# Kernel optimization log

Measured on AMD Instinct MI355X. Metric: run time of the kernel, lower is better.

The kernel has to match this reference:

```python
import jax, jax.numpy as jnp
import numpy as np
from functools import partial

NF, CD, NB = 64, 32, 3  # num_feat, chan_dyn, num_block


def _conv(x, w, b, stride, pad):
    out = jax.lax.conv_general_dilated(x, w, (stride, stride), ((pad, pad), (pad, pad)),
                                       dimension_numbers=('NCHW', 'OIHW', 'NCHW'))
    return out + b[None, :, None, None]


def _condition_tp(x, w1, b1, w2, b2, w3, b3):
    # ZeroPad2d(1) + conv(stride=2, pad=0) == conv with pad=1, stride=2
    h = jax.nn.relu(_conv(x, w1, b1, 2, 1))   # 7x7
    h = jax.nn.relu(_conv(h, w2, b2, 2, 1))   # 3x3
    h = jax.nn.relu(_conv(h, w3, b3, 2, 1))   # 3x3
    return h.mean(axis=(2, 3))                # [N, 32]


def _lstm_step(x, h, c, w):
    # ConvLSTMCell with 1x1 kernel on 1x1 spatial maps -> plain matmul
    gates = jnp.concatenate([x, h], axis=1) @ w.T        # [N, 4*NF]
    i, f, o, g = jnp.split(gates, 4, axis=1)
    c = jax.nn.sigmoid(f) * c + jax.nn.sigmoid(i) * jnp.tanh(g)
    h = jax.nn.sigmoid(o) * jnp.tanh(c)
    return h, c


def _forward(x, cond, rep_w1, rep_w2, lstm_fw_w, lstm_bw_w, lstm_conv_w, lstm_conv_b,
             conv_first_w, conv_first_b, bc1_w, bc1_b, bc2_w, bc2_b, bc3_w, bc3_b,
             bscale_w, bscale_b, bshift_w, bshift_b, bshare1_w, bshare1_b, bdyn1_w,
             bshare2_w, bshare2_b, bdyn2_w, fc1_w, fc1_b, fc2_w, fc2_b, fc3_w, fc3_b,
             fconv_w, fconv_b, fscale_w, fscale_b, fshift_w, fshift_b):
    lrelu = partial(jax.nn.leaky_relu, negative_slope=0.1)
    b = x.shape[0]
    # conv_represent -> [B, CD*NF] -> pseudo-batch [CD*B, NF] (spatial is 1x1)
    rep = (lrelu(cond @ rep_w1.T) @ rep_w2.T).reshape(b * CD, NF)
    # bidirectional ConvLSTM over 2*NB steps of the same input
    hf = cf = hb = cb = jnp.zeros_like(rep)
    ws_for, ws_back = [], []
    for _ in range(NB * 2):
        hf, cf = _lstm_step(rep, hf, cf, lstm_fw_w)
        ws_for.append(hf)
        hb, cb = _lstm_step(rep, hb, cb, lstm_bw_w)
        ws_back.append(hb)
    ws_back = ws_back[::-1]

    x1 = jnp.einsum('oc,bchw->bohw', conv_first_w, x) + conv_first_b[None, :, None, None]
    for j in range(NB):
        ow1 = (jnp.concatenate([ws_for[2 * j], ws_back[2 * j]], axis=1) @ lstm_conv_w[2 * j].T
               + lstm_conv_b[2 * j]).reshape(b, CD, NF)
        ow2 = (jnp.concatenate([ws_for[2 * j + 1], ws_back[2 * j + 1]], axis=1) @ lstm_conv_w[2 * j + 1].T
               + lstm_conv_b[2 * j + 1]).reshape(b, CD, NF)
        # res_model
        cond_out = _condition_tp(x1, bc1_w[j], bc1_b[j], bc2_w[j], bc2_b[j], bc3_w[j], bc3_b[j])
        scale = (cond_out @ bscale_w[j].T + bscale_b[j])[:, :, None, None]
        shift = (cond_out @ bshift_w[j].T + bshift_b[j])[:, :, None, None]
        # HDA_conv 1: per-sample dynamic 1x1 conv + shared 1x1 conv
        dyn1 = jnp.einsum('oc,boc,bchw->bohw', bdyn1_w[j], ow1, x1)
        share1 = jnp.einsum('oc,bchw->bohw', bshare1_w[j], x1) + bshare1_b[j][None, :, None, None]
        out = jnp.concatenate([dyn1, share1], axis=1)
        out = jax.nn.relu(out * scale + shift + out)
        # HDA_conv 2
        dyn2 = jnp.einsum('oc,boc,bchw->bohw', bdyn2_w[j], ow2, out)
        share2 = jnp.einsum('oc,bchw->bohw', bshare2_w[j], out) + bshare2_b[j][None, :, None, None]
        x1 = x1 + jnp.concatenate([dyn2, share2], axis=1)  # res_scale = 1
    # feature_mo
    cond_out = _condition_tp(x1, fc1_w, fc1_b, fc2_w, fc2_b, fc3_w, fc3_b)
    scale = (cond_out @ fscale_w.T + fscale_b)[:, :, None, None]
    shift = (cond_out @ fshift_w.T + fshift_b)[:, :, None, None]
    out = jnp.einsum('oc,bchw->bohw', fconv_w, x1) + fconv_b[None, :, None, None]
    return out * scale + shift + out


def setup_inputs() -> dict:
    key = jax.random.key(0)
    ctr = iter(range(1000))
    def p(shape, s=0.05):
        return jax.random.normal(jax.random.fold_in(key, next(ctr)), shape, dtype=jnp.float32) * s
    d = {}
    d['x'] = p((2, 3, 384, 640), 1.0)
    d['cond'] = p((2, 7680), 1.0)
    d['rep_w1'] = p((64, 7680)); d['rep_w2'] = p((2048, 64))
    d['lstm_fw_w'] = p((4 * NF, 2 * NF)); d['lstm_bw_w'] = p((4 * NF, 2 * NF))
    d['lstm_conv_w'] = p((2 * NB, NF, 2 * NF)); d['lstm_conv_b'] = p((2 * NB, NF))
    d['conv_first_w'] = p((NF, 3)); d['conv_first_b'] = p((NF,))
    d['bc1_w'] = p((NB, 32, 64, 7, 7)); d['bc1_b'] = p((NB, 32))
    d['bc2_w'] = p((NB, 32, 32, 3, 3)); d['bc2_b'] = p((NB, 32))
    d['bc3_w'] = p((NB, 32, 32, 3, 3)); d['bc3_b'] = p((NB, 32))
    d['bscale_w'] = p((NB, NF, 32)); d['bscale_b'] = p((NB, NF))
    d['bshift_w'] = p((NB, NF, 32)); d['bshift_b'] = p((NB, NF))
    d['bshare1_w'] = p((NB, CD, NF)); d['bshare1_b'] = p((NB, CD))
    d['bdyn1_w'] = p((NB, CD, NF))
    d['bshare2_w'] = p((NB, CD, NF)); d['bshare2_b'] = p((NB, CD))
    d['bdyn2_w'] = p((NB, CD, NF))
    d['fc1_w'] = p((32, 64, 7, 7)); d['fc1_b'] = p((32,))
    d['fc2_w'] = p((32, 32, 3, 3)); d['fc2_b'] = p((32,))
    d['fc3_w'] = p((32, 32, 3, 3)); d['fc3_b'] = p((32,))
    d['fconv_w'] = p((2, NF)); d['fconv_b'] = p((2,))
    d['fscale_w'] = p((2, 32)); d['fscale_b'] = p((2,))
    d['fshift_w'] = p((2, 32)); d['fshift_b'] = p((2,))
    return d


def reference(x, cond, rep_w1, rep_w2, lstm_fw_w, lstm_bw_w, lstm_conv_w, lstm_conv_b,
              conv_first_w, conv_first_b, bc1_w, bc1_b, bc2_w, bc2_b, bc3_w, bc3_b,
              bscale_w, bscale_b, bshift_w, bshift_b, bshare1_w, bshare1_b, bdyn1_w,
              bshare2_w, bshare2_b, bdyn2_w, fc1_w, fc1_b, fc2_w, fc2_b, fc3_w, fc3_b,
              fconv_w, fconv_b, fscale_w, fscale_b, fshift_w, fshift_b):
    return _forward(x, cond, rep_w1, rep_w2, lstm_fw_w, lstm_bw_w, lstm_conv_w, lstm_conv_b,
                    conv_first_w, conv_first_b, bc1_w, bc1_b, bc2_w, bc2_b, bc3_w, bc3_b,
                    bscale_w, bscale_b, bshift_w, bshift_b, bshare1_w, bshare1_b, bdyn1_w,
                    bshare2_w, bshare2_b, bdyn2_w, fc1_w, fc1_b, fc2_w, fc2_b, fc3_w, fc3_b,
                    fconv_w, fconv_b, fscale_w, fscale_b, fshift_w, fshift_b)
```

## Files before the change

kernel.cpp:

```cpp
#include <hip/hip_runtime.h>
#include <math.h>

#define HW 245760
#define H_IN 384
#define W_IN 640

#define X1_OFF   0UL
#define C1_OFF   31457280UL
#define C2_OFF   35324160UL
#define C3_OFF   36290880UL
#define T1_OFF   36536640UL
#define REP_OFF  36536768UL
#define GX_OFF   36540864UL
#define WSF_OFF  36573632UL
#define WSB_OFF  36598208UL
#define OW_OFF   36622784UL
#define CO_OFF   36647360UL
#define PAR_OFF  36647424UL
#define FP_OFF   36664192UL
#define P_W1T 0
#define P_W2T 8192
#define P_B1  16384
#define P_B2  16448
#define P_SC  16512
#define P_SH  16640

#define X1BF_BYTES_OFF 146656800UL
#define X1BF_BYTES     62914560UL
#define WBF_BYTES_OFF  (X1BF_BYTES_OFF + X1BF_BYTES)
#define WBF_BYTES      802816UL
#define REQ_BYTES      (WBF_BYTES_OFF + WBF_BYTES)

typedef short short8 __attribute__((ext_vector_type(8)));
typedef unsigned short ushort8_t __attribute__((ext_vector_type(8)));
typedef float f32x16 __attribute__((ext_vector_type(16)));

__device__ __forceinline__ float sigf(float x){ return 1.f/(1.f+expf(-x)); }

__device__ __forceinline__ unsigned short f2bf(float f){
  union { float f; unsigned u; } x; x.f = f;
  unsigned r = x.u + 0x7fffu + ((x.u >> 16) & 1u);
  return (unsigned short)(r >> 16);
}
__device__ __forceinline__ float bf2f(unsigned short u){
  union { unsigned u; float f; } x; x.u = ((unsigned)u) << 16; return x.f;
}

__global__ __launch_bounds__(256) void k_rep1(const float* __restrict__ cond,
                                              const float* __restrict__ w1,
                                              float* __restrict__ ws){
  const int gid = blockIdx.x*256 + threadIdx.x;
  const int o = gid >> 6;
  const int lane = gid & 63;
  const int r = o >> 6, oc = o & 63;
  const float4* c4 = (const float4*)(cond + r*7680);
  const float4* w4 = (const float4*)(w1 + oc*7680);
  float s = 0.f;
  #pragma unroll 6
  for (int i = lane; i < 1920; i += 64){
    float4 a = c4[i], b = w4[i];
    s += a.x*b.x + a.y*b.y + a.z*b.z + a.w*b.w;
  }
  #pragma unroll
  for (int off = 32; off; off >>= 1) s += __shfl_xor(s, off, 64);
  if (lane == 0) ws[T1_OFF + o] = s > 0.f ? s : 0.1f*s;
}

__global__ __launch_bounds__(256) void k_rep2(const float* __restrict__ w2,
                                              float* __restrict__ ws){
  int gid = blockIdx.x*256 + threadIdx.x;
  int r = gid >> 11, j = gid & 2047;
  const float* t1 = ws + T1_OFF + r*64;
  const float* wr = w2 + j*64;
  float s = 0.f;
  #pragma unroll
  for (int k=0;k<64;k++) s += t1[k]*wr[k];
  ws[REP_OFF + gid] = s;
}

__global__ __launch_bounds__(256) void k_gx(const float* __restrict__ wfw,
                                            const float* __restrict__ wbw,
                                            float* __restrict__ ws){
  int gid = blockIdx.x*256 + threadIdx.x;
  int dir = gid >> 14; int rem = gid & 16383;
  int r = rem >> 8; int m = rem & 255;
  const float* w = (dir ? wbw : wfw) + m*128;
  const float* rp = ws + REP_OFF + r*64;
  float s = 0.f;
  #pragma unroll
  for (int k=0;k<64;k++) s += rp[k]*w[k];
  ws[GX_OFF + gid] = s;
}

__global__ __launch_bounds__(256) void k_lstm(const float* __restrict__ wfw,
                                              const float* __restrict__ wbw,
                                              float* __restrict__ ws){
  const int rg = blockIdx.x, dir = blockIdx.y;
  const int tid = threadIdx.x;
  const int gi = tid >> 6, col = tid & 63;
  const float* w = dir ? wbw : wfw;
  const float* gx = ws + GX_OFF + (size_t)dir*16384;
  float* outp = ws + (dir ? WSB_OFF : WSF_OFF);
  float wr[64];
  const float4* wrow = (const float4*)(w + (gi*64+col)*128 + 64);
  #pragma unroll
  for (int k4=0;k4<16;k4++){
    float4 t = wrow[k4];
    wr[k4*4+0]=t.x; wr[k4*4+1]=t.y; wr[k4*4+2]=t.z; wr[k4*4+3]=t.w;
  }
  __shared__ __align__(16) float hl[512];
  __shared__ float gl[2048];
  hl[tid] = 0.f; hl[tid+256] = 0.f;
  float cs0 = 0.f, cs1 = 0.f;
  __syncthreads();
  for (int t=0;t<6;t++){
    float acc[8];
    #pragma unroll
    for (int r=0;r<8;r++) acc[r] = gx[(rg*8+r)*256 + gi*64 + col];
    #pragma unroll
    for (int r=0;r<8;r++){
      #pragma unroll
      for (int k4=0;k4<16;k4++){
        float4 h4 = *(const float4*)&hl[r*64 + k4*4];
        acc[r] += h4.x*wr[k4*4] + h4.y*wr[k4*4+1] + h4.z*wr[k4*4+2] + h4.w*wr[k4*4+3];
      }
    }
    #pragma unroll
    for (int r=0;r<8;r++) gl[r*256 + gi*64 + col] = acc[r];
    __syncthreads();
    {
      int r = tid >> 6, cc = tid & 63;
      float vi = gl[r*256+cc], vf = gl[r*256+64+cc], vo = gl[r*256+128+cc], vg = gl[r*256+192+cc];
      cs0 = sigf(vf)*cs0 + sigf(vi)*tanhf(vg);
      float h = sigf(vo)*tanhf(cs0);
      hl[r*64+cc] = h;
      outp[t*4096 + (rg*8+r)*64 + cc] = h;
    }
    {
      int cid = tid + 256; int r = cid >> 6, cc = cid & 63;
      float vi = gl[r*256+cc], vf = gl[r*256+64+cc], vo = gl[r*256+128+cc], vg = gl[r*256+192+cc];
      cs1 = sigf(vf)*cs1 + sigf(vi)*tanhf(vg);
      float h = sigf(vo)*tanhf(cs1);
      hl[r*64+cc] = h;
      outp[t*4096 + (rg*8+r)*64 + cc] = h;
    }
    __syncthreads();
  }
}

__global__ __launch_bounds__(256) void k_ow(const float* __restrict__ lcw,
                                            const float* __restrict__ lcb,
                                            float* __restrict__ ws){
  int gid = blockIdx.x*256 + threadIdx.x;
  int t = gid >> 12; int rem = gid & 4095;
  int r = rem >> 6; int cc = rem & 63;
  const float* wf = lcw + t*8192 + cc*128;
  const float* xf = ws + WSF_OFF + t*4096 + r*64;
  const float* xb = ws + WSB_OFF + (size_t)(5-t)*4096 + r*64;
  float s = lcb[t*64+cc];
  #pragma unroll
  for (int k=0;k<64;k++) s += xf[k]*wf[k];
  #pragma unroll
  for (int k=0;k<64;k++) s += xb[k]*wf[64+k];
  ws[OW_OFF + gid] = s;
}

__global__ __launch_bounds__(256) void k_convfirst(const float* __restrict__ x,
                                                   const float* __restrict__ cw,
                                                   const float* __restrict__ cb,
                                                   float* __restrict__ x1planar,
                                                   unsigned short* __restrict__ xbf){
  __shared__ float wsm[192];
  __shared__ float bsm[64];
  const int tid = threadIdx.x, blk = blockIdx.x;
  const int b = blk / 960;
  const int px = (blk % 960)*256 + tid;
  if (tid < 192) wsm[tid] = cw[tid];
  if (tid < 64)  bsm[tid] = cb[tid];
  __syncthreads();
  float x0 = x[(size_t)(b*3+0)*HW + px];
  float x1v = x[(size_t)(b*3+1)*HW + px];
  float x2 = x[(size_t)(b*3+2)*HW + px];
  float* o = x1planar ? (x1planar + (size_t)b*64*HW + px) : (float*)0;
  #pragma unroll
  for (int i=0;i<8;i++){
    ushort8_t u;
    #pragma unroll
    for (int j=0;j<8;j++){
      int oc = i*8+j;
      float v = bsm[oc] + wsm[oc*3]*x0 + wsm[oc*3+1]*x1v + wsm[oc*3+2]*x2;
      if (x1planar) o[(size_t)oc*HW] = v;
      u[j] = f2bf(v);
    }
    if (xbf)
      *(ushort8_t*)(xbf + (((size_t)(i>>1)*2 + b)*HW + px)*16 + (i&1)*8) = u;
  }
}

__global__ __launch_bounds__(256) void k_wbf(const float* __restrict__ bc1w,
                                             const float* __restrict__ fc1w,
                                             unsigned short* __restrict__ wbf){
  int e = blockIdx.x*256 + threadIdx.x;
  int s = e / 100352; int r = e - s*100352;
  int tap = r >> 11; int rem = r & 2047; int oc = rem >> 6; int ic = rem & 63;
  const float* src = (s < 3) ? (bc1w + (size_t)s*100352) : fc1w;
  wbf[e] = f2bf(src[((size_t)oc*64 + ic)*49 + tap]);
}

__global__ __launch_bounds__(512, 2) void k_conv7_mfma(
    const unsigned short* __restrict__ xbf,
    const unsigned short* __restrict__ wbf,
    const float* __restrict__ bias,
    float* __restrict__ out)
{
  __shared__ __align__(16) unsigned short inS[37*2*36*16];
  __shared__ __align__(16) unsigned short wS[49*32*16];
  const int tid = threadIdx.x;
  const int wv = tid >> 6, l = tid & 63;
  const int mrow = l & 31, khalf = l >> 5;
  const int wo0 = blockIdx.x * 32, ho0 = blockIdx.y * 16;
  const int b = blockIdx.z;
  const int r0 = 2*ho0 - 1;

  f32x16 acc0, acc1;
  #pragma unroll
  for (int i=0;i<16;i++){ acc0[i]=0.f; acc1[i]=0.f; }

  for (int kc = 0; kc < 4; ++kc){
    const unsigned short* xplane = xbf + ((size_t)(kc*2 + b))*HW*16;
    __syncthreads();
    for (int idx = tid; idx < 37*72*2; idx += 512){
      int half = idx & 1; int e = idx >> 1;
      int row = e / 72; int rem = e - row*72;
      int p = (rem >= 36) ? 1 : 0;
      int qi = rem - 36*p;
      int r = r0 + row;
      int col = 2*(qi + wo0 - 1) + p;
      uint4 v = make_uint4(0u,0u,0u,0u);
      if ((unsigned)r < 384u && (unsigned)col < 640u)
        v = *(const uint4*)(xplane + ((size_t)r*640 + col)*16 + half*8);
      *(uint4*)(inS + ((size_t)e*16 + half*8)) = v;
    }
    for (int idx = tid; idx < 49*32*2; idx += 512){
      int half = idx & 1; int e = idx >> 1;
      uint4 v = *(const uint4*)(wbf + ((size_t)e*64 + kc*16 + half*8));
      *(uint4*)(wS + ((size_t)e*16 + half*8)) = v;
    }
    __syncthreads();

    #pragma unroll
    for (int kw = 0; kw < 7; ++kw){
      const int p = (kw+1)&1;
      const int qoff = (kw - 1 - p)/2 + 1;
      const int abase = ((4*wv)*2 + p)*36 + qoff + mrow;
      short8 A_[9];
      #define LDA(rr) (*(const short8*)(inS + ((size_t)(abase + (rr)*72))*16 + khalf*8))
      #define LDB(KH) (*(const short8*)(wS + ((((KH)*7+kw)*32 + mrow)*16 + khalf*8)))
      #define MF(AV,BV,AC) AC = __builtin_amdgcn_mfma_f32_32x32x16_bf16(AV, BV, AC, 0, 0, 0)
      A_[0]=LDA(0); A_[1]=LDA(1); A_[2]=LDA(2); A_[3]=LDA(3); A_[4]=LDA(4);
      A_[5]=LDA(5); A_[6]=LDA(6); A_[7]=LDA(7); A_[8]=LDA(8);
      #pragma unroll
      for (int kh = 0; kh < 7; ++kh){
        short8 Bq = LDB(kh);
        MF(A_[kh],   Bq, acc0);
        MF(A_[kh+2], Bq, acc1);
      }
      #undef LDA
      #undef LDB
      #undef MF
    }
  }

  const float bv = bias[mrow];
  #pragma unroll
  for (int mt = 0; mt < 2; ++mt){
    int ho = ho0 + 2*wv + mt;
    if (ho >= 190) continue;
    f32x16 av = mt ? acc1 : acc0;
    float* orow = out + (((size_t)b*32 + mrow)*190 + ho)*318;
    #pragma unroll
    for (int r = 0; r < 16; ++r){
      int m = (r&3) + 8*(r>>2) + 4*khalf;
      int wo = wo0 + m;
      if (wo < 318) orow[wo] = fmaxf(av[r] + bv, 0.f);
    }
  }
}

__global__ __launch_bounds__(256) void k_conv7(const float* __restrict__ in,
                                               const float* __restrict__ w,
                                               const float* __restrict__ bias,
                                               float* __restrict__ out){
  __shared__ float patch[37*37];
  __shared__ __align__(16) float wl[49*32];
  const int tid = threadIdx.x;
  const int og = tid >> 5, s = tid & 31;
  const int sy = s >> 1, sx0 = (s & 1)*8;
  const int bx = blockIdx.x, by = blockIdx.y, b = blockIdx.z;
  const int ir0 = by*32 - 1, ic0 = bx*32 - 1;
  float acc[4][8];
  #pragma unroll
  for (int i=0;i<4;i++)
    #pragma unroll
    for (int k=0;k<8;k++) acc[i][k]=0.f;
  for (int c=0;c<64;c++){
    const float* src = in + (size_t)(b*64+c)*HW;
    for (int idx=tid; idx<1369; idx+=256){
      int r = idx/37; int cc = idx - r*37;
      int ir = ir0 + r, ic = ic0 + cc;
      float v = 0.f;
      if ((unsigned)ir < H_IN && (unsigned)ic < W_IN) v = src[ir*W_IN + ic];
      patch[idx] = v;
    }
    for (int idx=tid; idx<1568; idx+=256)
      wl[idx] = w[((size_t)(idx&31)*64 + c)*49 + (idx>>5)];
    __syncthreads();
    #pragma unroll
    for (int kh=0;kh<7;kh++){
      const float* prow = &patch[(2*sy+kh)*37 + 2*sx0];
      #pragma unroll
      for (int kw=0;kw<7;kw++){
        float4 wv = *(const float4*)&wl[(kh*7+kw)*32 + og*4];
        #pragma unroll
        for (int i=0;i<8;i++){
          float xv = prow[2*i + kw];
          acc[0][i] += wv.x*xv; acc[1][i] += wv.y*xv;
          acc[2][i] += wv.z*xv; acc[3][i] += wv.w*xv;
        }
      }
    }
    __syncthreads();
  }
  const int ho = by*16 + sy;
  if (ho < 190){
    #pragma unroll
    for (int oo=0;oo<4;oo++){
      int o = og*4+oo; float bb = bias[o];
      float* orow = out + ((size_t)(b*32+o)*190 + ho)*318 + bx*16 + sx0;
      #pragma unroll
      for (int i=0;i<8;i++){
        int wo = bx*16 + sx0 + i;
        if (wo < 318) orow[i] = fmaxf(acc[oo][i] + bb, 0.f);
      }
    }
  }
}

__global__ __launch_bounds__(256) void k_conv3_fast(const float* __restrict__ in,
                                                    const float* __restrict__ w,
                                                    const float* __restrict__ bias,
                                                    float* __restrict__ out,
                                                    int Hi, int Wi, int Ho, int Wo,
                                                    float* __restrict__ co_partial){
  __shared__ __align__(16) float wl[32*9*8];
  __shared__ float wsum[4][4];
  const int tid = threadIdx.x;
  const int b = blockIdx.z;
  const int oc0 = blockIdx.y * 8;
  for (int idx = tid; idx < 2304; idx += 256){
    int ol = idx & 7; int rest = idx >> 3;
    int ic = rest / 9, k = rest - ic*9;
    wl[idx] = w[((size_t)(oc0+ol)*32 + ic)*9 + k];
  }
  __syncthreads();
  const int pxl = tid & 127, ocg = tid >> 7;
  const int HoWo = Ho*Wo;
  const int opx = blockIdx.x*128 + pxl;
  float acc0=0.f, acc1=0.f, acc2=0.f, acc3=0.f;
  if (opx < HoWo){
    const int ho = opx / Wo, wo = opx - ho*Wo;
    const int ir0 = 2*ho - 1, ic0 = 2*wo - 1;
    const float* inb = in + (size_t)b*32*Hi*Wi;
    for (int c = 0; c < 32; ++c){
      const float* src = inb + (size_t)c*Hi*Wi;
      float xv[9];
      #pragma unroll
      for (int kh=0;kh<3;kh++){
        int ir = ir0 + kh;
        bool rok = (unsigned)ir < (unsigned)Hi;
        #pragma unroll
        for (int kw=0;kw<3;kw++){
          int icc = ic0 + kw;
          xv[kh*3+kw] = (rok && (unsigned)icc < (unsigned)Wi) ? src[ir*Wi + icc] : 0.f;
        }
      }
      const float* wc = &wl[c*72 + ocg*4];
      #pragma unroll
      for (int k=0;k<9;k++){
        float4 wa = *(const float4*)(wc + k*8);
        float x = xv[k];
        acc0 += wa.x*x; acc1 += wa.y*x; acc2 += wa.z*x; acc3 += wa.w*x;
      }
    }
    acc0 = fmaxf(acc0 + bias[oc0+ocg*4+0], 0.f);
    acc1 = fmaxf(acc1 + bias[oc0+ocg*4+1], 0.f);
    acc2 = fmaxf(acc2 + bias[oc0+ocg*4+2], 0.f);
    acc3 = fmaxf(acc3 + bias[oc0+ocg*4+3], 0.f);
    if (!co_partial){
      float* ob = out + ((size_t)(b*32 + oc0 + ocg*4))*HoWo + opx;
      ob[0] = acc0;
      ob[(size_t)HoWo] = acc1;
      ob[(size_t)2*HoWo] = acc2;
      ob[(size_t)3*HoWo] = acc3;
    }
  }
  if (co_partial){
    float r0=acc0, r1=acc1, r2=acc2, r3=acc3;
    #pragma unroll
    for (int off=32; off; off>>=1){
      r0 += __shfl_xor(r0, off, 64);
      r1 += __shfl_xor(r1, off, 64);
      r2 += __shfl_xor(r2, off, 64);
      r3 += __shfl_xor(r3, off, 64);
    }
    int wvid = tid >> 6;
    if ((tid & 63) == 0){
      wsum[wvid][0]=r0; wsum[wvid][1]=r1; wsum[wvid][2]=r2; wsum[wvid][3]=r3;
    }
    __syncthreads();
    if (tid < 8){
      int i = tid & 3; int pair = tid >> 2;
      float v = wsum[pair*2][i] + wsum[pair*2+1][i];
      co_partial[(size_t)blockIdx.x*64 + b*32 + oc0 + pair*4 + i] = v;
    }
  }
}

__global__ __launch_bounds__(256) void k_mkparams(const float* __restrict__ bsw, const float* __restrict__ bsb,
                                                  const float* __restrict__ bhw, const float* __restrict__ bhb,
                                                  const float* __restrict__ dyn1, const float* __restrict__ sh1w, const float* __restrict__ sh1b,
                                                  const float* __restrict__ dyn2, const float* __restrict__ sh2w, const float* __restrict__ sh2b,
                                                  int j2, float* __restrict__ ws,
                                                  unsigned short* __restrict__ w1oc,
                                                  unsigned short* __restrict__ w2oc){
  const int bid = blockIdx.x;
  const int tid = threadIdx.x;
  float* P = ws + PAR_OFF;
  if (bid < 16){
    const float* ow1 = ws + OW_OFF + (size_t)j2*4096;
    const float* ow2 = ws + OW_OFF + (size_t)(j2+1)*4096;
    for (int idx = bid*256 + tid; idx < 8192; idx += 4096){
      int b = idx>>12, rem = idx&4095, c = rem>>6, o = rem&63;
      float v1, v2;
      if (o < 32){
        v1 = dyn1[o*64+c]*ow1[(b*32+o)*64+c];
        v2 = dyn2[o*64+c]*ow2[(b*32+o)*64+c];
      } else {
        v1 = sh1w[(o-32)*64+c];
        v2 = sh2w[(o-32)*64+c];
      }
      P[P_W1T + idx] = v1;
      P[P_W2T + idx] = v2;
      int t = b*4096 + o*64 + c;
      w1oc[t] = f2bf(v1);
      w2oc[t] = f2bf(v2);
    }
  } else {
    __shared__ float coL[64];
    const float* part = ws + GX_OFF;
    if (tid < 64){
      float s = 0.f;
      for (int bx=0;bx<30;bx++) s += part[bx*64 + tid];
      coL[tid] = s * (1.f/3840.f);
    }
    __syncthreads();
    if (tid < 128){
      int b = tid>>6, o = tid&63;
      float s = bsb[o];
      #pragma unroll
      for (int k=0;k<32;k++) s += coL[b*32+k]*bsw[o*32+k];
      P[P_SC + tid] = 1.f + s;
    } else {
      int t2 = tid-128; int b = t2>>6, o = t2&63;
      float s = bhb[o];
      #pragma unroll
      for (int k=0;k<32;k++) s += coL[b*32+k]*bhw[o*32+k];
      P[P_SH + t2] = s;
    }
    if (tid < 64){
      P[P_B1+tid] = (tid<32) ? 0.f : sh1b[tid-32];
      P[P_B2+tid] = (tid<32) ? 0.f : sh2b[tid-32];
    }
  }
}

__global__ __launch_bounds__(256, 4) void k_pointwise_mfma(
    const float* __restrict__ ws,
    const unsigned short* __restrict__ w1oc,
    const unsigned short* __restrict__ w2oc,
    unsigned short* __restrict__ xbf)
{
  __shared__ float scs[64], shs[64], b1s[64], b2s[64];
  __shared__ __align__(16) uint4 outbuf[2048];
  const int tid = threadIdx.x;
  const int blk = blockIdx.x;
  const int b = blk / 960;
  const int px0 = (blk % 960) * 256;
  const float* P = ws + PAR_OFF;
  if (tid < 64){
    scs[tid] = P[P_SC + b*64 + tid];
    shs[tid] = P[P_SH + b*64 + tid];
    b1s[tid] = P[P_B1 + tid];
    b2s[tid] = P[P_B2 + tid];
  }
  __syncthreads();
  const int wv = tid >> 6, l = tid & 63;
  const int lane31 = l & 31, myh = l >> 5;
  const unsigned short* w1g = w1oc + (size_t)b*4096;
  const unsigned short* w2g = w2oc + (size_t)b*4096;

  #pragma unroll
  for (int nt = 0; nt < 2; ++nt){
    const int pxl = wv*64 + nt*32 + lane31;
    const int mypx = px0 + pxl;
    short8 Bsave[4];
    f32x16 a1_0, a1_1;
    #pragma unroll
    for (int i=0;i<16;i++){ a1_0[i]=0.f; a1_1[i]=0.f; }
    #pragma unroll
    for (int kc=0;kc<4;kc++){
      short8 Bx = *(const short8*)(xbf + ((size_t)(kc*2+b)*HW + mypx)*16 + myh*8);
      Bsave[kc] = Bx;
      short8 A0 = *(const short8*)(w1g + (size_t)lane31*64 + kc*16 + myh*8);
      short8 A1 = *(const short8*)(w1g + (size_t)(32+lane31)*64 + kc*16 + myh*8);
      a1_0 = __builtin_amdgcn_mfma_f32_32x32x16_bf16(A0, Bx, a1_0, 0, 0, 0);
      a1_1 = __builtin_amdgcn_mfma_f32_32x32x16_bf16(A1, Bx, a1_1, 0, 0, 0);
    }
    unsigned hp0[8], hp1[8];
    #pragma unroll
    for (int mt=0;mt<2;mt++){
      #pragma unroll
      for (int p=0;p<8;p++){
        unsigned half0=0, half1=0;
        #pragma unroll
        for (int e=0;e<2;e++){
          int reg = 2*p+e;
          int o1 = mt*32 + (reg&3) + 8*(reg>>2) + 4*myh;
          float v = mt ? a1_1[reg] : a1_0[reg];
          float t = (v + b1s[o1]) * scs[o1] + shs[o1];
          t = fmaxf(t, 0.f);
          if (e) half1 = f2bf(t); else half0 = f2bf(t);
        }
        unsigned pk = half0 | (half1<<16);
        if (mt) hp1[p] = pk; else hp0[p] = pk;
      }
    }
    f32x16 a2_0, a2_1;
    #pragma unroll
    for (int i=0;i<16;i++){ a2_0[i]=0.f; a2_1[i]=0.f; }
    #pragma unroll
    for (int kc=0;kc<4;kc++){
      const int base = 4*(kc&1);
      unsigned e0,e1,e2,e3;
      if (kc < 2){ e0=hp0[base+0]; e1=hp0[base+1]; e2=hp0[base+2]; e3=hp0[base+3]; }
      else       { e0=hp1[base+0]; e1=hp1[base+1]; e2=hp1[base+2]; e3=hp1[base+3]; }
      unsigned sA = myh ? e0 : e2;
      unsigned sB = myh ? e1 : e3;
      unsigned rA = __shfl_xor(sA, 32, 64);
      unsigned rB = __shfl_xor(sB, 32, 64);
      union { unsigned u[4]; short8 s; } Bh;
      Bh.u[0] = myh ? rA : e0;
      Bh.u[1] = myh ? rB : e1;
      Bh.u[2] = myh ? e2 : rA;
      Bh.u[3] = myh ? e3 : rB;
      short8 A0 = *(const short8*)(w2g + (size_t)lane31*64 + kc*16 + myh*8);
      short8 A1 = *(const short8*)(w2g + (size_t)(32+lane31)*64 + kc*16 + myh*8);
      a2_0 = __builtin_amdgcn_mfma_f32_32x32x16_bf16(A0, Bh.s, a2_0, 0, 0, 0);
      a2_1 = __builtin_amdgcn_mfma_f32_32x32x16_bf16(A1, Bh.s, a2_1, 0, 0, 0);
    }
    #pragma unroll
    for (int mt2=0;mt2<2;mt2++){
      #pragma unroll
      for (int q=0;q<4;q++){
        float d[4], p[4];
        #pragma unroll
        for (int e=0;e<4;e++){
          int reg = 4*q+e;
          int ch = mt2*32 + e + 8*q + 4*myh;
          d[e] = (mt2 ? a2_1[reg] : a2_0[reg]) + b2s[ch];
        }
        #pragma unroll
        for (int e=0;e<4;e++) p[e] = __shfl_xor(d[e], 32, 64);
        if (myh == (q & 1)){
          float row8[8];
          #pragma unroll
          for (int e=0;e<4;e++){
            row8[e]   = myh ? p[e] : d[e];
            row8[4+e] = myh ? d[e] : p[e];
          }
          union { short8 s; unsigned short us[8]; } oldv;
          oldv.s = Bsave[2*mt2 + (q>>1)];
          unsigned w[4];
          #pragma unroll
          for (int k=0;k<4;k++){
            float n0 = bf2f(oldv.us[2*k+0]) + row8[2*k+0];
            float n1 = bf2f(oldv.us[2*k+1]) + row8[2*k+1];
            w[k] = (unsigned)f2bf(n0) | ((unsigned)f2bf(n1) << 16);
          }
          int slot = mt2*4 + q;
          outbuf[pxl*8 + ((slot + pxl) & 7)] = make_uint4(w[0],w[1],w[2],w[3]);
        }
      }
    }
  }
  __syncthreads();
  uint4* gout = (uint4*)xbf;
  #pragma unroll
  for (int k=0;k<8;k++){
    int idx = tid + k*256;
    int plane = idx >> 9, rem = idx & 511;
    int pxl = rem >> 1, half = rem & 1;
    int slot = plane*2 + half;
    gout[((size_t)(plane*2+b)*HW + px0 + pxl)*2 + half] = outbuf[pxl*8 + ((slot + pxl) & 7)];
  }
}

#define FMA4(A,W,X) { A.x += (W)*(X).x; A.y += (W)*(X).y; A.z += (W)*(X).z; A.w += (W)*(X).w; }
__global__ __launch_bounds__(128) void k_pointwise(float* __restrict__ ws){
  __shared__ __align__(16) float xt[64*128];
  __shared__ __align__(16) float wt[64*64];
  __shared__ float b1s[64], b2s[64], scs[64], shs[64];
  const int tid = threadIdx.x;
  const int blk = blockIdx.x;
  const int b = blk / 1920;
  const int px0 = (blk % 1920) * 128;
  float* x1 = ws + X1_OFF;
  const float* P = ws + PAR_OFF;
  const float4* xg = (const float4*)(x1 + (size_t)b*64*HW + px0);
  float4* xt4 = (float4*)xt;
  float4* wt4 = (float4*)wt;
  for (int idx=tid; idx<2048; idx+=128){
    int c = idx>>5, p4 = idx&31;
    xt4[c*32 + (p4&3)*8 + (p4>>2)] = xg[(size_t)c*(HW/4) + p4];
  }
  const float4* w1g = (const float4*)(P + P_W1T + b*4096);
  for (int idx=tid; idx<1024; idx+=128) wt4[idx] = w1g[idx];
  if (tid < 64){
    b1s[tid]=P[P_B1+tid]; b2s[tid]=P[P_B2+tid];
    scs[tid]=P[P_SC + b*64 + tid]; shs[tid]=P[P_SH + b*64 + tid];
  }
  __syncthreads();
  const int og = tid>>3, pg = tid&7, o0 = og*4;
  float4 a[4][4];
  #pragma unroll
  for (int oo=0;oo<4;oo++){
    float bv = b1s[o0+oo];
    a[oo][0]=a[oo][1]=a[oo][2]=a[oo][3]=make_float4(bv,bv,bv,bv);
  }
  for (int c=0;c<64;c++){
    float4 wv = wt4[c*16 + og];
    float4 x0 = xt4[c*32 + pg];
    float4 x1q = xt4[c*32 + 8 + pg];
    float4 x2 = xt4[c*32 + 16 + pg];
    float4 x3 = xt4[c*32 + 24 + pg];
    FMA4(a[0][0],wv.x,x0); FMA4(a[0][1],wv.x,x1q); FMA4(a[0][2],wv.x,x2); FMA4(a[0][3],wv.x,x3);
    FMA4(a[1][0],wv.y,x0); FMA4(a[1][1],wv.y,x1q); FMA4(a[1][2],wv.y,x2); FMA4(a[1][3],wv.y,x3);
    FMA4(a[2][0],wv.z,x0); FMA4(a[2][1],wv.z,x1q); FMA4(a[2][2],wv.z,x2); FMA4(a[2][3],wv.z,x3);
    FMA4(a[3][0],wv.w,x0); FMA4(a[3][1],wv.w,x1q); FMA4(a[3][2],wv.w,x2); FMA4(a[3][3],wv.w,x3);
  }
  #pragma unroll
  for (int oo=0;oo<4;oo++){
    float sc = scs[o0+oo], sh = shs[o0+oo];
    #pragma unroll
    for (int q=0;q<4;q++){
      a[oo][q].x = fmaxf(a[oo][q].x*sc + sh, 0.f);
      a[oo][q].y = fmaxf(a[oo][q].y*sc + sh, 0.f);
      a[oo][q].z = fmaxf(a[oo][q].z*sc + sh, 0.f);
      a[oo][q].w = fmaxf(a[oo][q].w*sc + sh, 0.f);
    }
  }
  __syncthreads();
  #pragma unroll
  for (int oo=0;oo<4;oo++)
    #pragma unroll
    for (int q=0;q<4;q++)
      xt4[(o0+oo)*32 + q*8 + pg] = a[oo][q];
  const float4* w2g = (const float4*)(P + P_W2T + b*4096);
  for (int idx=tid; idx<1024; idx+=128) wt4[idx] = w2g[idx];
  __syncthreads();
  #pragma unroll
  for (int oo=0;oo<4;oo++){
    float bv = b2s[o0+oo];
    a[oo][0]=a[oo][1]=a[oo][2]=a[oo][3]=make_float4(bv,bv,bv,bv);
  }
  for (int c=0;c<64;c++){
    float4 wv = wt4[c*16 + og];
    float4 x0 = xt4[c*32 + pg];
    float4 x1q = xt4[c*32 + 8 + pg];
    float4 x2 = xt4[c*32 + 16 + pg];
    float4 x3 = xt4[c*32 + 24 + pg];
    FMA4(a[0][0],wv.x,x0); FMA4(a[0][1],wv.x,x1q); FMA4(a[0][2],wv.x,x2); FMA4(a[0][3],wv.x,x3);
    FMA4(a[1][0],wv.y,x0); FMA4(a[1][1],wv.y,x1q); FMA4(a[1][2],wv.y,x2); FMA4(a[1][3],wv.y,x3);
    FMA4(a[2][0],wv.z,x0); FMA4(a[2][1],wv.z,x1q); FMA4(a[2][2],wv.z,x2); FMA4(a[2][3],wv.z,x3);
    FMA4(a[3][0],wv.w,x0); FMA4(a[3][1],wv.w,x1q); FMA4(a[3][2],wv.w,x2); FMA4(a[3][3],wv.w,x3);
  }
  #pragma unroll
  for (int q=0;q<4;q++){
    #pragma unroll
    for (int oo=0;oo<4;oo++){
      float4* xo = (float4*)(x1 + (size_t)(b*64 + o0+oo)*HW + px0);
      float4 old = xo[pg*4 + q];
      old.x += a[oo][q].x; old.y += a[oo][q].y; old.z += a[oo][q].z; old.w += a[oo][q].w;
      xo[pg*4 + q] = old;
    }
  }
}

__global__ void k_mkfinal(const float* __restrict__ fsw, const float* __restrict__ fsb,
                          const float* __restrict__ fhw, const float* __restrict__ fhb,
                          float* __restrict__ ws){
  __shared__ float coL[64];
  const float* part = ws + GX_OFF;
  int tid = threadIdx.x;
  if (tid < 64){
    float s = 0.f;
    for (int bx=0;bx<30;bx++) s += part[bx*64 + tid];
    coL[tid] = s * (1.f/3840.f);
  }
  __syncthreads();
  if (tid < 4){
    int b = tid>>1, o = tid&1;
    const float* co = coL + b*32;
    float s = fsb[o], h = fhb[o];
    for (int k=0;k<32;k++){ s += co[k]*fsw[o*32+k]; h += co[k]*fhw[o*32+k]; }
    ws[FP_OFF + tid] = 1.f + s;
    ws[FP_OFF + 4 + tid] = h;
  }
}

__global__ __launch_bounds__(256) void k_final_bf(const float* __restrict__ fw,
                                                  const float* __restrict__ fb,
                                                  const float* __restrict__ ws,
                                                  const unsigned short* __restrict__ xbf,
                                                  float* __restrict__ out){
  __shared__ float w[128];
  __shared__ float pr[8];
  __shared__ float bb[2];
  const int tid = threadIdx.x, blk = blockIdx.x;
  const int b = blk / 960;
  const int px = (blk % 960)*256 + tid;
  if (tid < 128) w[tid] = fw[tid];
  if (tid < 8)   pr[tid] = ws[FP_OFF + tid];
  if (tid < 2)   bb[tid] = fb[tid];
  __syncthreads();
  float a0 = bb[0], a1 = bb[1];
  #pragma unroll
  for (int p=0;p<4;p++){
    const unsigned short* row = xbf + ((size_t)(p*2+b)*HW + px)*16;
    #pragma unroll
    for (int hh=0;hh<2;hh++){
      union { uint4 v; unsigned short us[8]; } u;
      u.v = *(const uint4*)(row + hh*8);
      #pragma unroll
      for (int j=0;j<8;j++){
        int c = p*16 + hh*8 + j;
        float f = bf2f(u.us[j]);
        a0 += w[c]*f; a1 += w[64+c]*f;
      }
    }
  }
  out[((size_t)b*2+0)*HW + px] = a0*pr[b*2+0] + pr[4 + b*2+0];
  out[((size_t)b*2+1)*HW + px] = a1*pr[b*2+1] + pr[4 + b*2+1];
}

__global__ __launch_bounds__(256) void k_final(const float* __restrict__ fw,
                                               const float* __restrict__ fb,
                                               const float* __restrict__ ws,
                                               float* __restrict__ out){
  __shared__ float w[128];
  __shared__ float pr[8];
  __shared__ float bb[2];
  const int tid = threadIdx.x, blk = blockIdx.x;
  const int b = blk / 960;
  const int px = (blk % 960)*256 + tid;
  if (tid < 128) w[tid] = fw[tid];
  if (tid < 8)   pr[tid] = ws[FP_OFF + tid];
  if (tid < 2)   bb[tid] = fb[tid];
  __syncthreads();
  const float* xp = ws + X1_OFF + (size_t)b*64*HW + px;
  float a0 = bb[0], a1 = bb[1];
  #pragma unroll
  for (int c=0;c<64;c++){
    float xv = xp[(size_t)c*HW];
    a0 += w[c]*xv; a1 += w[64+c]*xv;
  }
  out[((size_t)b*2+0)*HW + px] = a0*pr[b*2+0] + pr[4 + b*2+0];
  out[((size_t)b*2+1)*HW + px] = a1*pr[b*2+1] + pr[4 + b*2+1];
}

extern "C" void kernel_launch(void* const* d_in, const int* in_sizes, int n_in,
                              void* d_out, int out_size, void* d_ws, size_t ws_size,
                              hipStream_t stream) {
  const float* x            = (const float*)d_in[0];
  const float* cond         = (const float*)d_in[1];
  const float* rep_w1       = (const float*)d_in[2];
  const float* rep_w2       = (const float*)d_in[3];
  const float* lstm_fw_w    = (const float*)d_in[4];
  const float* lstm_bw_w    = (const float*)d_in[5];
  const float* lstm_conv_w  = (const float*)d_in[6];
  const float* lstm_conv_b  = (const float*)d_in[7];
  const float* conv_first_w = (const float*)d_in[8];
  const float* conv_first_b = (const float*)d_in[9];
  const float* bc1_w  = (const float*)d_in[10];
  const float* bc1_b  = (const float*)d_in[11];
  const float* bc2_w  = (const float*)d_in[12];
  const float* bc2_b  = (const float*)d_in[13];
  const float* bc3_w  = (const float*)d_in[14];
  const float* bc3_b  = (const float*)d_in[15];
  const float* bscale_w = (const float*)d_in[16];
  const float* bscale_b = (const float*)d_in[17];
  const float* bshift_w = (const float*)d_in[18];
  const float* bshift_b = (const float*)d_in[19];
  const float* bshare1_w = (const float*)d_in[20];
  const float* bshare1_b = (const float*)d_in[21];
  const float* bdyn1_w   = (const float*)d_in[22];
  const float* bshare2_w = (const float*)d_in[23];
  const float* bshare2_b = (const float*)d_in[24];
  const float* bdyn2_w   = (const float*)d_in[25];
  const float* fc1_w = (const float*)d_in[26];
  const float* fc1_b = (const float*)d_in[27];
  const float* fc2_w = (const float*)d_in[28];
  const float* fc2_b = (const float*)d_in[29];
  const float* fc3_w = (const float*)d_in[30];
  const float* fc3_b = (const float*)d_in[31];
  const float* fconv_w  = (const float*)d_in[32];
  const float* fconv_b  = (const float*)d_in[33];
  const float* fscale_w = (const float*)d_in[34];
  const float* fscale_b = (const float*)d_in[35];
  const float* fshift_w = (const float*)d_in[36];
  const float* fshift_b = (const float*)d_in[37];

  float* ws = (float*)d_ws;
  const bool use_mfma = (ws_size >= REQ_BYTES);
  unsigned short* xbf = use_mfma ? (unsigned short*)((char*)d_ws + X1BF_BYTES_OFF) : (unsigned short*)0;
  unsigned short* wbf = (unsigned short*)((char*)d_ws + WBF_BYTES_OFF);
  unsigned short* w1oc = (unsigned short*)((char*)d_ws + C1_OFF*4UL);
  unsigned short* w2oc = w1oc + 8192;
  float* copart = ws + GX_OFF;

  k_rep1<<<32, 256, 0, stream>>>(cond, rep_w1, ws);
  k_rep2<<<16, 256, 0, stream>>>(rep_w2, ws);
  k_gx<<<128, 256, 0, stream>>>(lstm_fw_w, lstm_bw_w, ws);
  k_lstm<<<dim3(8,2), 256, 0, stream>>>(lstm_fw_w, lstm_bw_w, ws);
  k_ow<<<96, 256, 0, stream>>>(lstm_conv_w, lstm_conv_b, ws);
  if (use_mfma)
    k_wbf<<<1568, 256, 0, stream>>>(bc1_w, fc1_w, wbf);
  k_convfirst<<<1920, 256, 0, stream>>>(x, conv_first_w, conv_first_b,
                                        use_mfma ? (float*)0 : (ws + X1_OFF), xbf);

  for (int j = 0; j < 3; j++){
    if (use_mfma){
      k_conv7_mfma<<<dim3(10,12,2), 512, 0, stream>>>(xbf, wbf + (size_t)j*100352, bc1_b + j*32, ws + C1_OFF);
    } else {
      k_conv7<<<dim3(20,12,2), 256, 0, stream>>>(ws + X1_OFF, bc1_w + (size_t)j*32*64*49, bc1_b + j*32, ws + C1_OFF);
    }
    k_conv3_fast<<<dim3(119,4,2), 256, 0, stream>>>(ws + C1_OFF, bc2_w + (size_t)j*32*32*9, bc2_b + j*32, ws + C2_OFF, 190, 318, 95, 159, (float*)0);
    k_conv3_fast<<<dim3(30,4,2), 256, 0, stream>>>(ws + C2_OFF, bc3_w + (size_t)j*32*32*9, bc3_b + j*32, ws + C3_OFF, 95, 159, 48, 80, copart);
    k_mkparams<<<17, 256, 0, stream>>>(bscale_w + j*2048, bscale_b + j*64,
                                      bshift_w + j*2048, bshift_b + j*64,
                                      bdyn1_w + j*2048, bshare1_w + j*2048, bshare1_b + j*32,
                                      bdyn2_w + j*2048, bshare2_w + j*2048, bshare2_b + j*32,
                                      2*j, ws, w1oc, w2oc);
    if (use_mfma)
      k_pointwise_mfma<<<1920, 256, 0, stream>>>(ws, w1oc, w2oc, xbf);
    else
      k_pointwise<<<3840, 128, 0, stream>>>(ws);
  }

  if (use_mfma){
    k_conv7_mfma<<<dim3(10,12,2), 512, 0, stream>>>(xbf, wbf + (size_t)3*100352, fc1_b, ws + C1_OFF);
  } else {
    k_conv7<<<dim3(20,12,2), 256, 0, stream>>>(ws + X1_OFF, fc1_w, fc1_b, ws + C1_OFF);
  }
  k_conv3_fast<<<dim3(119,4,2), 256, 0, stream>>>(ws + C1_OFF, fc2_w, fc2_b, ws + C2_OFF, 190, 318, 95, 159, (float*)0);
  k_conv3_fast<<<dim3(30,4,2), 256, 0, stream>>>(ws + C2_OFF, fc3_w, fc3_b, ws + C3_OFF, 95, 159, 48, 80, copart);
  k_mkfinal<<<1, 64, 0, stream>>>(fscale_w, fscale_b, fshift_w, fshift_b, ws);
  if (use_mfma)
    k_final_bf<<<1920, 256, 0, stream>>>(fconv_w, fconv_b, ws, xbf, (float*)d_out);
  else
    k_final<<<1920, 256, 0, stream>>>(fconv_w, fconv_b, ws, (float*)d_out);
}
```

Before: 686.8 us.

## Shrink conv7 MFMA tile and split weight staging into two kh phases

The 7x7 MFMA convolution now uses 256-thread blocks that each cover 8 output rows instead of 16, which doubles the grid. Shared memory drops because the input tile holds 21 rows and the weight buffer holds only 4 of the 7 kh taps at a time. The remaining 3 taps are loaded in a second phase guarded by extra barriers. This is meant to raise occupancy and the number of blocks in flight, at the cost of more redundant input-halo loads and extra synchronisation per channel chunk.

```diff
diff --git a/kernel.cpp b/kernel.cpp
--- a/kernel.cpp
+++ b/kernel.cpp
@@ -207,18 +207,18 @@
   wbf[e] = f2bf(src[((size_t)oc*64 + ic)*49 + tap]);
 }
 
-__global__ __launch_bounds__(512, 2) void k_conv7_mfma(
+__global__ __launch_bounds__(256) void k_conv7_mfma(
     const unsigned short* __restrict__ xbf,
     const unsigned short* __restrict__ wbf,
     const float* __restrict__ bias,
     float* __restrict__ out)
 {
-  __shared__ __align__(16) unsigned short inS[37*2*36*16];
-  __shared__ __align__(16) unsigned short wS[49*32*16];
+  __shared__ __align__(16) unsigned short inS[21*2*36*16];
+  __shared__ __align__(16) unsigned short wS[28*32*16];
   const int tid = threadIdx.x;
   const int wv = tid >> 6, l = tid & 63;
   const int mrow = l & 31, khalf = l >> 5;
-  const int wo0 = blockIdx.x * 32, ho0 = blockIdx.y * 16;
+  const int wo0 = blockIdx.x * 32, ho0 = blockIdx.y * 8;
   const int b = blockIdx.z;
   const int r0 = 2*ho0 - 1;
 
@@ -229,7 +229,7 @@
   for (int kc = 0; kc < 4; ++kc){
     const unsigned short* xplane = xbf + ((size_t)(kc*2 + b))*HW*16;
     __syncthreads();
-    for (int idx = tid; idx < 37*72*2; idx += 512){
+    for (int idx = tid; idx < 21*72*2; idx += 256){
       int half = idx & 1; int e = idx >> 1;
       int row = e / 72; int rem = e - row*72;
       int p = (rem >= 36) ? 1 : 0;
@@ -241,7 +241,7 @@
         v = *(const uint4*)(xplane + ((size_t)r*640 + col)*16 + half*8);
       *(uint4*)(inS + ((size_t)e*16 + half*8)) = v;
     }
-    for (int idx = tid; idx < 49*32*2; idx += 512){
+    for (int idx = tid; idx < 28*32*2; idx += 256){
       int half = idx & 1; int e = idx >> 1;
       uint4 v = *(const uint4*)(wbf + ((size_t)e*64 + kc*16 + half*8));
       *(uint4*)(wS + ((size_t)e*16 + half*8)) = v;
@@ -253,20 +253,46 @@
       const int p = (kw+1)&1;
       const int qoff = (kw - 1 - p)/2 + 1;
       const int abase = ((4*wv)*2 + p)*36 + qoff + mrow;
-      short8 A_[9];
+      short8 A_[6];
       #define LDA(rr) (*(const short8*)(inS + ((size_t)(abase + (rr)*72))*16 + khalf*8))
-      #define LDB(KH) (*(const short8*)(wS + ((((KH)*7+kw)*32 + mrow)*16 + khalf*8)))
+      #define LDBA(KH) (*(const short8*)(wS + ((((KH)*7+kw)*32 + mrow)*16 + khalf*8)))
+      #define MF(AV,BV,AC) AC = __builtin_amdgcn_mfma_f32_32x32x16_bf16(AV, BV, AC, 0, 0, 0)
+      A_[0]=LDA(0); A_[1]=LDA(1); A_[2]=LDA(2); A_[3]=LDA(3); A_[4]=LDA(4); A_[5]=LDA(5);
+      #pragma unroll
+      for (int kh = 0; kh < 4; ++kh){
+        short8 Bq = LDBA(kh);
+        MF(A_[kh],   Bq, acc0);
+        MF(A_[kh+2], Bq, acc1);
+      }
+      #undef LDA
+      #undef LDBA
+      #undef MF
+    }
+    __syncthreads();
+    for (int idx = tid; idx < 21*32*2; idx += 256){
+      int half = idx & 1; int e = idx >> 1;
+      uint4 v = *(const uint4*)(wbf + ((size_t)(e + 28*32)*64 + kc*16 + half*8));
+      *(uint4*)(wS + ((size_t)e*16 + half*8)) = v;
+    }
+    __syncthreads();
+    #pragma unroll
+    for (int kw = 0; kw < 7; ++kw){
+      const int p = (kw+1)&1;
+      const int qoff = (kw - 1 - p)/2 + 1;
+      const int abase = ((4*wv)*2 + p)*36 + qoff + mrow;
+      short8 A_[5];
+      #define LDA(rr) (*(const short8*)(inS + ((size_t)(abase + (4+(rr))*72))*16 + khalf*8))
+      #define LDBB(KH) (*(const short8*)(wS + ((((KH)*7+kw)*32 + mrow)*16 + khalf*8)))
       #define MF(AV,BV,AC) AC = __builtin_amdgcn_mfma_f32_32x32x16_bf16(AV, BV, AC, 0, 0, 0)
       A_[0]=LDA(0); A_[1]=LDA(1); A_[2]=LDA(2); A_[3]=LDA(3); A_[4]=LDA(4);
-      A_[5]=LDA(5); A_[6]=LDA(6); A_[7]=LDA(7); A_[8]=LDA(8);
-      #pragma unroll
-      for (int kh = 0; kh < 7; ++kh){
-        short8 Bq = LDB(kh);
+      #pragma unroll
+      for (int kh = 0; kh < 3; ++kh){
+        short8 Bq = LDBB(kh);
         MF(A_[kh],   Bq, acc0);
         MF(A_[kh+2], Bq, acc1);
       }
       #undef LDA
-      #undef LDB
+      #undef LDBB
       #undef MF
     }
   }
@@ -850,7 +876,7 @@
 
   for (int j = 0; j < 3; j++){
     if (use_mfma){
-      k_conv7_mfma<<<dim3(10,12,2), 512, 0, stream>>>(xbf, wbf + (size_t)j*100352, bc1_b + j*32, ws + C1_OFF);
+      k_conv7_mfma<<<dim3(10,24,2), 256, 0, stream>>>(xbf, wbf + (size_t)j*100352, bc1_b + j*32, ws + C1_OFF);
     } else {
       k_conv7<<<dim3(20,12,2), 256, 0, stream>>>(ws + X1_OFF, bc1_w + (size_t)j*32*64*49, bc1_b + j*32, ws + C1_OFF);
     }
@@ -868,7 +894,7 @@
   }
 
   if (use_mfma){
-    k_conv7_mfma<<<dim3(10,12,2), 512, 0, stream>>>(xbf, wbf + (size_t)3*100352, fc1_b, ws + C1_OFF);
+    k_conv7_mfma<<<dim3(10,24,2), 256, 0, stream>>>(xbf, wbf + (size_t)3*100352, fc1_b, ws + C1_OFF);
   } else {
     k_conv7<<<dim3(20,12,2), 256, 0, stream>>>(ws + X1_OFF, fc1_w, fc1_b, ws + C1_OFF);
   }
```

After: 692.1 us. About the same (+0.8%).
